# Optimization experiments

Measured on AMD Instinct MI355X. Metric: run time of the kernel, lower is better.

The kernel has to match this reference:

```python
import jax, jax.numpy as jnp
import numpy as np

S, N, H, O = 128, 2048, 128, 128  # seq_len(=input_size), num_samples, hidden_size, output_size


def setup_inputs() -> dict:
    key = jax.random.key(0)
    ks = jax.random.split(key, 7)
    scale = 1.0 / np.sqrt(H)
    u = lambda k, shp: jax.random.uniform(k, shp, jnp.float32, -scale, scale)
    return {
        "x": jax.random.normal(ks[0], (S, N, H), jnp.float32),
        "W_ih": u(ks[1], (4 * H, H)),   # PyTorch gate order: i, f, g, o
        "W_hh": u(ks[2], (4 * H, H)),
        "b_ih": u(ks[3], (4 * H,)),
        "b_hh": u(ks[4], (4 * H,)),
        "W_out": u(ks[5], (O, H)),
        "b_out": u(ks[6], (O,)),
    }


def _lstm_forward(x, W_ih, W_hh, b_ih, b_hh, W_out, b_out):
    n, h = x.shape[1], W_hh.shape[1]
    # Precompute input contribution to gates for all timesteps: [S, N, 4H]
    xg = jnp.einsum("snh,gh->sng", x, W_ih) + (b_ih + b_hh)

    def step(carry, xt):
        h_t, c_t = carry
        gates = xt + h_t @ W_hh.T  # [N, 4H]
        i, f, g, o = jnp.split(gates, 4, axis=-1)
        i = jax.nn.sigmoid(i)
        f = jax.nn.sigmoid(f)
        g = jnp.tanh(g)
        o = jax.nn.sigmoid(o)
        c_t = f * c_t + i * g
        h_t = o * jnp.tanh(c_t)
        return (h_t, c_t), h_t

    h0 = jnp.zeros((n, h), x.dtype)  # init_hidden(): zeros
    c0 = jnp.zeros((n, h), x.dtype)
    _, out = jax.lax.scan(step, (h0, c0), xg)  # out: [S, N, H]
    # Linear projection fused over all timesteps
    pred = jnp.einsum("snh,oh->sno", out, W_out) + b_out  # [S, N, O]
    return pred


def reference(x, W_ih, W_hh, b_ih, b_hh, W_out, b_out):
    return _lstm_forward(x, W_ih, W_hh, b_ih, b_hh, W_out, b_out)
```

## Files before the change

kernel.cpp:

```cpp
#include <hip/hip_runtime.h>
#include <hip/hip_bf16.h>


#define S_LEN   128
#define N_BATCH 2048
#define H_DIM   128
#define O_DIM   128

using short8  = __attribute__((ext_vector_type(8))) short;
using floatx4 = __attribute__((ext_vector_type(4))) float;
typedef unsigned short u16;

#define ROWP     264
#define BUFELEMS (16 * ROWP)

__device__ __forceinline__ u16 f2b(float f) {
    unsigned int u = __float_as_uint(f);
    return (u16)((u + 0x7FFF + ((u >> 16) & 1)) >> 16);
}
__device__ __forceinline__ short8 pack8(const float* p) {
    short8 r;
#pragma unroll
    for (int i = 0; i < 8; ++i) r[i] = (short)f2b(p[i]);
    return r;
}
__device__ __forceinline__ float sigmoidf_fast(float v) {
    return __builtin_amdgcn_rcpf(1.0f + __builtin_amdgcn_exp2f(-1.4426950408889634f * v));
}
__device__ __forceinline__ float tanhf_fast(float v) {
    return 1.0f - 2.0f * __builtin_amdgcn_rcpf(1.0f + __builtin_amdgcn_exp2f(2.8853900817779268f * v));
}

__global__ __launch_bounds__(512, 2)
void lstm_persist(const float* __restrict__ x,
                  const float* __restrict__ W_ih,
                  const float* __restrict__ W_hh,
                  const float* __restrict__ b_ih,
                  const float* __restrict__ b_hh,
                  const float* __restrict__ W_out,
                  const float* __restrict__ b_out,
                  float* __restrict__ pred) {
    __shared__ short sh[2 * BUFELEMS];

    const int tid  = (int)threadIdx.x;
    const int wave = tid >> 6;
    const int lane = tid & 63;
    const int quad = lane >> 4;
    const int l15  = lane & 15;
    const int n0   = (int)blockIdx.x * 16;

    short8 wg[4][8];
    float  biasv[4];
#pragma unroll
    for (int t = 0; t < 4; ++t) {
        const int g = t * 128 + wave * 16 + l15;
#pragma unroll
        for (int kk = 0; kk < 4; ++kk)
            wg[t][kk] = pack8(W_ih + g * H_DIM + kk * 32 + quad * 8);
#pragma unroll
        for (int kk = 4; kk < 8; ++kk)
            wg[t][kk] = pack8(W_hh + g * H_DIM + (kk - 4) * 32 + quad * 8);
        biasv[t] = b_ih[g] + b_hh[g];
    }
    short8 wo[4];
    const int ocol = wave * 16 + l15;
#pragma unroll
    for (int kk = 0; kk < 4; ++kk)
        wo[kk] = pack8(W_out + ocol * H_DIM + kk * 32 + quad * 8);
    const float bo = b_out[ocol];

    for (int i = tid; i < 16 * 128; i += 512)
        sh[(i >> 7) * ROWP + 128 + (i & 127)] = 0;

    const int  xm = tid >> 4;
    const int  xc = (tid & 15) * 8;
    const bool isLoader = (tid < 256);
    if (isLoader) {
        const float* p = x + ((size_t)(n0 + xm)) * H_DIM + xc;
        float4 f0 = *reinterpret_cast<const float4*>(p);
        float4 f1 = *reinterpret_cast<const float4*>(p + 4);
        float tmp[8] = {f0.x, f0.y, f0.z, f0.w, f1.x, f1.y, f1.z, f1.w};
        *reinterpret_cast<short8*>(&sh[xm * ROWP + xc]) = pack8(tmp);
    }

    float cc[4] = {0.f, 0.f, 0.f, 0.f};
    __syncthreads();

    const int arow = l15 * ROWP + quad * 8;
    const int hcol = 128 + wave * 16 + l15;

    for (int s = 0; s < S_LEN; ++s) {
        short* shb = sh + (s & 1) * BUFELEMS;
        short* shn = sh + ((s & 1) ^ 1) * BUFELEMS;

        float4 xr0, xr1;
        const bool doLoad = isLoader && (s + 1 < S_LEN);
        if (doLoad) {
            const float* p = x + ((size_t)(s + 1) * N_BATCH + n0 + xm) * H_DIM + xc;
            xr0 = *reinterpret_cast<const float4*>(p);
            xr1 = *reinterpret_cast<const float4*>(p + 4);
        }

        floatx4 acc0 = {biasv[0], biasv[0], biasv[0], biasv[0]};
        floatx4 acc1 = {biasv[1], biasv[1], biasv[1], biasv[1]};
        floatx4 acc2 = {biasv[2], biasv[2], biasv[2], biasv[2]};
        floatx4 acc3 = {biasv[3], biasv[3], biasv[3], biasv[3]};
        floatx4 ao   = {bo, bo, bo, bo};

#pragma unroll
        for (int kk = 0; kk < 8; ++kk) {
            short8 a = *reinterpret_cast<const short8*>(&shb[arow + kk * 32]);
            acc0 = __builtin_amdgcn_mfma_f32_16x16x32_bf16(a, wg[0][kk], acc0, 0, 0, 0);
            acc1 = __builtin_amdgcn_mfma_f32_16x16x32_bf16(a, wg[1][kk], acc1, 0, 0, 0);
            acc2 = __builtin_amdgcn_mfma_f32_16x16x32_bf16(a, wg[2][kk], acc2, 0, 0, 0);
            acc3 = __builtin_amdgcn_mfma_f32_16x16x32_bf16(a, wg[3][kk], acc3, 0, 0, 0);
            if (kk >= 4)
                ao = __builtin_amdgcn_mfma_f32_16x16x32_bf16(a, wo[kk - 4], ao, 0, 0, 0);
        }

        if (s > 0) {
            size_t base = ((size_t)(s - 1) * N_BATCH + n0 + quad * 4) * O_DIM + wave * 16 + l15;
#pragma unroll
            for (int r = 0; r < 4; ++r)
                pred[base + (size_t)r * O_DIM] = ao[r];
        }

        float hv[4];
#pragma unroll
        for (int r = 0; r < 4; ++r) {
            float iv = sigmoidf_fast(acc0[r]);
            float fv = sigmoidf_fast(acc1[r]);
            float gv = tanhf_fast(acc2[r]);
            float ov = sigmoidf_fast(acc3[r]);
            cc[r] = fv * cc[r] + iv * gv;
            hv[r] = ov * tanhf_fast(cc[r]);
        }

        if (doLoad) {
            float tmp[8] = {xr0.x, xr0.y, xr0.z, xr0.w, xr1.x, xr1.y, xr1.z, xr1.w};
            *reinterpret_cast<short8*>(&shn[xm * ROWP + xc]) = pack8(tmp);
        }
#pragma unroll
        for (int r = 0; r < 4; ++r)
            shn[(quad * 4 + r) * ROWP + hcol] = (short)f2b(hv[r]);

        __syncthreads();
    }

    floatx4 ao = {bo, bo, bo, bo};
#pragma unroll
    for (int kk = 4; kk < 8; ++kk) {
        short8 a = *reinterpret_cast<const short8*>(&sh[arow + kk * 32]);
        ao = __builtin_amdgcn_mfma_f32_16x16x32_bf16(a, wo[kk - 4], ao, 0, 0, 0);
    }
    size_t base = ((size_t)(S_LEN - 1) * N_BATCH + n0 + quad * 4) * O_DIM + wave * 16 + l15;
#pragma unroll
    for (int r = 0; r < 4; ++r)
        pred[base + (size_t)r * O_DIM] = ao[r];
}

extern "C" void kernel_launch(void* const* d_in, const int* in_sizes, int n_in,
                              void* d_out, int out_size, void* d_ws, size_t ws_size,
                              hipStream_t stream) {
    const float* x    = (const float*)d_in[0];
    const float* Wih  = (const float*)d_in[1];
    const float* Whh  = (const float*)d_in[2];
    const float* bih  = (const float*)d_in[3];
    const float* bhh  = (const float*)d_in[4];
    const float* Wout = (const float*)d_in[5];
    const float* bout = (const float*)d_in[6];
    float* pred = (float*)d_out;

    lstm_persist<<<dim3(N_BATCH / 16), dim3(512), 0, stream>>>(
        x, Wih, Whh, bih, bhh, Wout, bout, pred);
}
```

Before: 380.0 us.

## Software-pipeline input-gate MFMAs one step ahead of the recurrent critical path

Splits the fused 8-chunk gate GEMM into a recurrent-only part (W_hh on h) and an input part (W_ih on x). The x contribution for step s+1 is computed during step s, after the recurrent MFMAs and before the activations, so each step's serial dependency on h only covers 4 k-chunks. The x prefetch now runs two steps ahead with all 512 threads loading float4, which spreads load latency. The cost is more live accumulator registers (extra xg vectors, split weight arrays) under a 512-thread, 2-blocks-per-CU launch bound, so spills or lower occupancy are possible.

```diff
diff --git a/kernel.cpp b/kernel.cpp
--- a/kernel.cpp
+++ b/kernel.cpp
@@ -8,6 +8,7 @@
 #define O_DIM   128
 
 using short8  = __attribute__((ext_vector_type(8))) short;
+using short4v = __attribute__((ext_vector_type(4))) short;
 using floatx4 = __attribute__((ext_vector_type(4))) float;
 typedef unsigned short u16;
 
@@ -22,6 +23,12 @@
     short8 r;
 #pragma unroll
     for (int i = 0; i < 8; ++i) r[i] = (short)f2b(p[i]);
+    return r;
+}
+__device__ __forceinline__ short4v pack4(float4 f) {
+    short4v r;
+    r[0] = (short)f2b(f.x); r[1] = (short)f2b(f.y);
+    r[2] = (short)f2b(f.z); r[3] = (short)f2b(f.w);
     return r;
 }
 __device__ __forceinline__ float sigmoidf_fast(float v) {
@@ -49,73 +56,73 @@
     const int l15  = lane & 15;
     const int n0   = (int)blockIdx.x * 16;
 
-    short8 wg[4][8];
+    short8 wx[4][4], wh[4][4], wo[4];
     float  biasv[4];
 #pragma unroll
     for (int t = 0; t < 4; ++t) {
         const int g = t * 128 + wave * 16 + l15;
 #pragma unroll
-        for (int kk = 0; kk < 4; ++kk)
-            wg[t][kk] = pack8(W_ih + g * H_DIM + kk * 32 + quad * 8);
-#pragma unroll
-        for (int kk = 4; kk < 8; ++kk)
-            wg[t][kk] = pack8(W_hh + g * H_DIM + (kk - 4) * 32 + quad * 8);
+        for (int kk = 0; kk < 4; ++kk) {
+            wx[t][kk] = pack8(W_ih + g * H_DIM + kk * 32 + quad * 8);
+            wh[t][kk] = pack8(W_hh + g * H_DIM + kk * 32 + quad * 8);
+        }
         biasv[t] = b_ih[g] + b_hh[g];
     }
-    short8 wo[4];
     const int ocol = wave * 16 + l15;
 #pragma unroll
     for (int kk = 0; kk < 4; ++kk)
         wo[kk] = pack8(W_out + ocol * H_DIM + kk * 32 + quad * 8);
     const float bo = b_out[ocol];
 
+    const int xm = tid >> 5;
+    const int xq = (tid & 31) * 4;
+
     for (int i = tid; i < 16 * 128; i += 512)
         sh[(i >> 7) * ROWP + 128 + (i & 127)] = 0;
-
-    const int  xm = tid >> 4;
-    const int  xc = (tid & 15) * 8;
-    const bool isLoader = (tid < 256);
-    if (isLoader) {
-        const float* p = x + ((size_t)(n0 + xm)) * H_DIM + xc;
-        float4 f0 = *reinterpret_cast<const float4*>(p);
-        float4 f1 = *reinterpret_cast<const float4*>(p + 4);
-        float tmp[8] = {f0.x, f0.y, f0.z, f0.w, f1.x, f1.y, f1.z, f1.w};
-        *reinterpret_cast<short8*>(&sh[xm * ROWP + xc]) = pack8(tmp);
+    {
+        float4 f0 = *reinterpret_cast<const float4*>(x + ((size_t)(n0 + xm)) * H_DIM + xq);
+        float4 f1 = *reinterpret_cast<const float4*>(x + ((size_t)N_BATCH + n0 + xm) * H_DIM + xq);
+        *reinterpret_cast<short4v*>(&sh[BUFELEMS + xm * ROWP + xq]) = pack4(f0);
+        *reinterpret_cast<short4v*>(&sh[xm * ROWP + xq]) = pack4(f1);
     }
-
-    float cc[4] = {0.f, 0.f, 0.f, 0.f};
+    float4 xcur = *reinterpret_cast<const float4*>(x + ((size_t)2 * N_BATCH + n0 + xm) * H_DIM + xq);
+    float4 xnext = *reinterpret_cast<const float4*>(x + ((size_t)3 * N_BATCH + n0 + xm) * H_DIM + xq);
     __syncthreads();
 
     const int arow = l15 * ROWP + quad * 8;
     const int hcol = 128 + wave * 16 + l15;
 
+    floatx4 xg0 = {biasv[0], biasv[0], biasv[0], biasv[0]};
+    floatx4 xg1 = {biasv[1], biasv[1], biasv[1], biasv[1]};
+    floatx4 xg2 = {biasv[2], biasv[2], biasv[2], biasv[2]};
+    floatx4 xg3 = {biasv[3], biasv[3], biasv[3], biasv[3]};
+#pragma unroll
+    for (int kk = 0; kk < 4; ++kk) {
+        short8 a = *reinterpret_cast<const short8*>(&sh[BUFELEMS + arow + kk * 32]);
+        xg0 = __builtin_amdgcn_mfma_f32_16x16x32_bf16(a, wx[0][kk], xg0, 0, 0, 0);
+        xg1 = __builtin_amdgcn_mfma_f32_16x16x32_bf16(a, wx[1][kk], xg1, 0, 0, 0);
+        xg2 = __builtin_amdgcn_mfma_f32_16x16x32_bf16(a, wx[2][kk], xg2, 0, 0, 0);
+        xg3 = __builtin_amdgcn_mfma_f32_16x16x32_bf16(a, wx[3][kk], xg3, 0, 0, 0);
+    }
+    __syncthreads();
+
+    float cc[4] = {0.f, 0.f, 0.f, 0.f};
+
     for (int s = 0; s < S_LEN; ++s) {
         short* shb = sh + (s & 1) * BUFELEMS;
         short* shn = sh + ((s & 1) ^ 1) * BUFELEMS;
 
-        float4 xr0, xr1;
-        const bool doLoad = isLoader && (s + 1 < S_LEN);
-        if (doLoad) {
-            const float* p = x + ((size_t)(s + 1) * N_BATCH + n0 + xm) * H_DIM + xc;
-            xr0 = *reinterpret_cast<const float4*>(p);
-            xr1 = *reinterpret_cast<const float4*>(p + 4);
-        }
-
-        floatx4 acc0 = {biasv[0], biasv[0], biasv[0], biasv[0]};
-        floatx4 acc1 = {biasv[1], biasv[1], biasv[1], biasv[1]};
-        floatx4 acc2 = {biasv[2], biasv[2], biasv[2], biasv[2]};
-        floatx4 acc3 = {biasv[3], biasv[3], biasv[3], biasv[3]};
-        floatx4 ao   = {bo, bo, bo, bo};
+        floatx4 g0 = xg0, g1 = xg1, g2 = xg2, g3 = xg3;
+        floatx4 ao = {bo, bo, bo, bo};
 
 #pragma unroll
-        for (int kk = 0; kk < 8; ++kk) {
-            short8 a = *reinterpret_cast<const short8*>(&shb[arow + kk * 32]);
-            acc0 = __builtin_amdgcn_mfma_f32_16x16x32_bf16(a, wg[0][kk], acc0, 0, 0, 0);
-            acc1 = __builtin_amdgcn_mfma_f32_16x16x32_bf16(a, wg[1][kk], acc1, 0, 0, 0);
-            acc2 = __builtin_amdgcn_mfma_f32_16x16x32_bf16(a, wg[2][kk], acc2, 0, 0, 0);
-            acc3 = __builtin_amdgcn_mfma_f32_16x16x32_bf16(a, wg[3][kk], acc3, 0, 0, 0);
-            if (kk >= 4)
-                ao = __builtin_amdgcn_mfma_f32_16x16x32_bf16(a, wo[kk - 4], ao, 0, 0, 0);
+        for (int kk = 0; kk < 4; ++kk) {
+            short8 ah = *reinterpret_cast<const short8*>(&shb[arow + 128 + kk * 32]);
+            g0 = __builtin_amdgcn_mfma_f32_16x16x32_bf16(ah, wh[0][kk], g0, 0, 0, 0);
+            g1 = __builtin_amdgcn_mfma_f32_16x16x32_bf16(ah, wh[1][kk], g1, 0, 0, 0);
+            g2 = __builtin_amdgcn_mfma_f32_16x16x32_bf16(ah, wh[2][kk], g2, 0, 0, 0);
+            g3 = __builtin_amdgcn_mfma_f32_16x16x32_bf16(ah, wh[3][kk], g3, 0, 0, 0);
+            ao = __builtin_amdgcn_mfma_f32_16x16x32_bf16(ah, wo[kk], ao, 0, 0, 0);
         }
 
         if (s > 0) {
@@ -125,33 +132,48 @@
                 pred[base + (size_t)r * O_DIM] = ao[r];
         }
 
+        xg0 = floatx4{biasv[0], biasv[0], biasv[0], biasv[0]};
+        xg1 = floatx4{biasv[1], biasv[1], biasv[1], biasv[1]};
+        xg2 = floatx4{biasv[2], biasv[2], biasv[2], biasv[2]};
+        xg3 = floatx4{biasv[3], biasv[3], biasv[3], biasv[3]};
+#pragma unroll
+        for (int kk = 0; kk < 4; ++kk) {
+            short8 axv = *reinterpret_cast<const short8*>(&shb[arow + kk * 32]);
+            xg0 = __builtin_amdgcn_mfma_f32_16x16x32_bf16(axv, wx[0][kk], xg0, 0, 0, 0);
+            xg1 = __builtin_amdgcn_mfma_f32_16x16x32_bf16(axv, wx[1][kk], xg1, 0, 0, 0);
+            xg2 = __builtin_amdgcn_mfma_f32_16x16x32_bf16(axv, wx[2][kk], xg2, 0, 0, 0);
+            xg3 = __builtin_amdgcn_mfma_f32_16x16x32_bf16(axv, wx[3][kk], xg3, 0, 0, 0);
+        }
+
+        if (s <= 125)
+            *reinterpret_cast<short4v*>(&shn[xm * ROWP + xq]) = pack4(xcur);
+        if (s <= 124)
+            xnext = *reinterpret_cast<const float4*>(
+                x + ((size_t)(s + 3) * N_BATCH + n0 + xm) * H_DIM + xq);
+
         float hv[4];
 #pragma unroll
         for (int r = 0; r < 4; ++r) {
-            float iv = sigmoidf_fast(acc0[r]);
-            float fv = sigmoidf_fast(acc1[r]);
-            float gv = tanhf_fast(acc2[r]);
-            float ov = sigmoidf_fast(acc3[r]);
+            float iv = sigmoidf_fast(g0[r]);
+            float fv = sigmoidf_fast(g1[r]);
+            float gv = tanhf_fast(g2[r]);
+            float ov = sigmoidf_fast(g3[r]);
             cc[r] = fv * cc[r] + iv * gv;
             hv[r] = ov * tanhf_fast(cc[r]);
-        }
-
-        if (doLoad) {
-            float tmp[8] = {xr0.x, xr0.y, xr0.z, xr0.w, xr1.x, xr1.y, xr1.z, xr1.w};
-            *reinterpret_cast<short8*>(&shn[xm * ROWP + xc]) = pack8(tmp);
         }
 #pragma unroll
         for (int r = 0; r < 4; ++r)
             shn[(quad * 4 + r) * ROWP + hcol] = (short)f2b(hv[r]);
 
+        xcur = xnext;
         __syncthreads();
     }
 
     floatx4 ao = {bo, bo, bo, bo};
 #pragma unroll
-    for (int kk = 4; kk < 8; ++kk) {
-        short8 a = *reinterpret_cast<const short8*>(&sh[arow + kk * 32]);
-        ao = __builtin_amdgcn_mfma_f32_16x16x32_bf16(a, wo[kk - 4], ao, 0, 0, 0);
+    for (int kk = 0; kk < 4; ++kk) {
+        short8 ah = *reinterpret_cast<const short8*>(&sh[arow + 128 + kk * 32]);
+        ao = __builtin_amdgcn_mfma_f32_16x16x32_bf16(ah, wo[kk], ao, 0, 0, 0);
     }
     size_t base = ((size_t)(S_LEN - 1) * N_BATCH + n0 + quad * 4) * O_DIM + wave * 16 + l15;
 #pragma unroll
```

Measured after the change: 359.9 us. 5.3% less time.
